# Performance work log

Hardware: AMD Instinct MI355X
Metric: run time of the kernel (lower is better)

The kernel has to match this reference:

```python
import jax, jax.numpy as jnp
import numpy as np


def _gru_layer(x_seq, W_ih, W_hh, b_ih, b_hh):
    """PyTorch-semantics GRU layer. x_seq: [T, B, in]. Returns outputs [T, B, H]."""
    H = W_hh.shape[1]
    # Precompute input projections for all timesteps: [T, B, 3H]
    xg = jnp.einsum('tbi,gi->tbg', x_seq, W_ih) + b_ih

    def step(h, xg_t):
        hg = h @ W_hh.T + b_hh                      # [B, 3H]
        xr, xz, xn = jnp.split(xg_t, 3, axis=-1)    # gate order: r, z, n
        hr, hz, hn = jnp.split(hg, 3, axis=-1)
        r = jax.nn.sigmoid(xr + hr)
        z = jax.nn.sigmoid(xz + hz)
        n = jnp.tanh(xn + r * hn)
        h_new = (1.0 - z) * n + z * h
        return h_new, h_new

    h0 = jnp.zeros((x_seq.shape[1], H), dtype=x_seq.dtype)
    _, out = jax.lax.scan(step, h0, xg)
    return out


def setup_inputs() -> dict:
    key = jax.random.key(0)
    ks = jax.random.split(key, 12)
    T, B, I, H, O = 128, 2048, 18, 256, 4
    s = 0.05  # small init scale to avoid gate saturation
    return {
        'x':     jax.random.normal(ks[0], (T, B, I), dtype=jnp.float32),
        'W_ih0': jax.random.normal(ks[1], (3 * H, I), dtype=jnp.float32) * s,
        'W_hh0': jax.random.normal(ks[2], (3 * H, H), dtype=jnp.float32) * s,
        'b_ih0': jax.random.normal(ks[3], (3 * H,), dtype=jnp.float32) * s,
        'b_hh0': jax.random.normal(ks[4], (3 * H,), dtype=jnp.float32) * s,
        'W_ih1': jax.random.normal(ks[5], (3 * H, H), dtype=jnp.float32) * s,
        'W_hh1': jax.random.normal(ks[6], (3 * H, H), dtype=jnp.float32) * s,
        'b_ih1': jax.random.normal(ks[7], (3 * H,), dtype=jnp.float32) * s,
        'b_hh1': jax.random.normal(ks[8], (3 * H,), dtype=jnp.float32) * s,
        'fc_w':  jax.random.normal(ks[9], (O, H), dtype=jnp.float32) * s,
        'fc_b':  jax.random.normal(ks[10], (O,), dtype=jnp.float32) * s,
    }


def reference(x, W_ih0, W_hh0, b_ih0, b_hh0, W_ih1, W_hh1, b_ih1, b_hh1, fc_w, fc_b):
    h1 = _gru_layer(x, W_ih0, W_hh0, b_ih0, b_hh0)   # [T, B, H]
    h2 = _gru_layer(h1, W_ih1, W_hh1, b_ih1, b_hh1)  # [T, B, H]
    logits = h2[-1] @ fc_w.T + fc_b                  # [B, O]
    return jax.nn.sigmoid(logits) * 2.0 - 1.0
```

## Files before the change

### kernel.cpp

```cpp
#include <hip/hip_runtime.h>
#include <hip/hip_bf16.h>
#include <stdint.h>

#define T_STEPS 128
#define BATCH   2048
#define IN_DIM  18
#define HID     256

#define NT   48
#define KT0  9
#define KT1  16
#define L0_FRAGS 432
#define L1_FRAGS 768
#define TOT_FRAGS 1200

#define CNT_OFF  1310720u
#define CNTA(g)  (CNT_OFF + (uint32_t)(g) * 64u)
#define CNTB(g)  (CNT_OFF + 4096u + (uint32_t)(g) * 64u)
#define CNTC(g)  (CNT_OFF + 8192u + (uint32_t)(g) * 64u)
#define H1_OFF   1441792u
#define H1SLOT(t, g) (H1_OFF + (uint32_t)(((((t) & 3) * 64) + (g)) * 16384))
#define XG_OFF   5898240u
#define XGSLOT(t, g) (XG_OFF + (uint32_t)(((((t) & 3) * 64) + (g)) * 49152))

#define XGOFFS(col, inner) ((uint32_t)((col) * 64 + ((inner) ^ (((col) & 7) << 3))))

using frag_ab = __attribute__((ext_vector_type(8))) short;
using f32x4   = __attribute__((ext_vector_type(4))) float;
using uint4v  = __attribute__((ext_vector_type(4))) unsigned int;
using uint2v  = __attribute__((ext_vector_type(2))) unsigned int;

__device__ __forceinline__ unsigned short f2bf(float f) {
  unsigned int u = __float_as_uint(f);
  u = (u + 0x7fffu + ((u >> 16) & 1u)) >> 16;
  return (unsigned short)u;
}
__device__ __forceinline__ float bf2f(unsigned short v) {
  return __uint_as_float((uint32_t)v << 16);
}
__device__ __forceinline__ float sigmoidf_(float v) {
  return __builtin_amdgcn_rcpf(1.f + __expf(-v));
}
__device__ __forceinline__ float tanhf_(float v) {
  float a = fabsf(v);
  float e = __expf(-2.f * a);
  float r = (1.f - e) * __builtin_amdgcn_rcpf(1.f + e);
  return v < 0.f ? -r : r;
}
__device__ __forceinline__ f32x4 mfma16(frag_ab a, frag_ab b, f32x4 c) {
  return __builtin_amdgcn_mfma_f32_16x16x32_bf16(a, b, c, 0, 0, 0);
}

__global__ __launch_bounds__(256) void repack_w(
    const float* __restrict__ Wih0, const float* __restrict__ Whh0,
    const float* __restrict__ Wih1, const float* __restrict__ Whh1,
    unsigned short* __restrict__ wq)
{
  int g = blockIdx.x * 256 + threadIdx.x;
  if (g >= TOT_FRAGS * 64) return;
  int f = g >> 6;
  int L = g & 63;
  int q = L >> 4, c16 = L & 15;
  unsigned short v[8];
  if (f < L0_FRAGS) {
    int n = f / KT0, kt = f - n * KT0;
    int col = n * 16 + c16;
    if (kt == 0) {
      #pragma unroll
      for (int j = 0; j < 8; ++j) {
        int k = q * 8 + j;
        v[j] = (k < IN_DIM) ? f2bf(Wih0[col * IN_DIM + k]) : (unsigned short)0;
      }
    } else {
      int kb = (kt - 1) * 32 + q * 8;
      #pragma unroll
      for (int j = 0; j < 8; ++j) v[j] = f2bf(Whh0[col * HID + kb + j]);
    }
  } else {
    int f1 = f - L0_FRAGS;
    int n = f1 / KT1, kt = f1 - n * KT1;
    int col = n * 16 + c16;
    const float* __restrict__ W = (kt < 8) ? Wih1 : Whh1;
    int kb = (kt & 7) * 32 + q * 8;
    #pragma unroll
    for (int j = 0; j < 8; ++j) v[j] = f2bf(W[col * HID + kb + j]);
  }
  frag_ab pv;
  #pragma unroll
  for (int j = 0; j < 8; ++j) pv[j] = (short)v[j];
  *(frag_ab*)((char*)wq + ((size_t)f << 10) + (size_t)(L << 4)) = pv;
}

__global__ __launch_bounds__(256) void clear_cnt(uint32_t* __restrict__ c) {
  int i = blockIdx.x * 256 + threadIdx.x;
  if (i < 3072) c[i] = 0;
}

__global__ __launch_bounds__(1024) void gru_pipe(
    const float* __restrict__ x,
    const float* __restrict__ bih0, const float* __restrict__ bhh0,
    const float* __restrict__ bih1, const float* __restrict__ bhh1,
    const float* __restrict__ fcw,  const float* __restrict__ fcb,
    char* __restrict__ ws,
    float* __restrict__ out)
{
  __shared__ __align__(16) char smem[82944];

  const int tid  = threadIdx.x;
  const int wave = tid >> 6;
  const int lane = tid & 63;
  const int q    = lane >> 4;
  const int c16  = lane & 15;
  const int bid  = blockIdx.x;
  const uint32_t lane16 = (uint32_t)(lane << 4);
  int dead = 0;

#define BARRIER() asm volatile("s_waitcnt lgkmcnt(0)\n\ts_barrier" ::: "memory")
#define ISSUE3(sl, oR, oZ, oN)                                              \
  asm volatile("global_load_dwordx4 %0, %3, %6\n\t"                         \
               "global_load_dwordx4 %1, %4, %6\n\t"                         \
               "global_load_dwordx4 %2, %5, %6"                             \
               : "=&v"(rr_[sl]), "=&v"(rz_[sl]), "=&v"(rn_[sl])             \
               : "v"((uint32_t)(oR)), "v"((uint32_t)(oZ)),                  \
                 "v"((uint32_t)(oN)), "s"(ws)                               \
               : "memory")
#define WAIT3(sl, NSTR)                                                     \
  asm volatile("s_waitcnt vmcnt(" NSTR ")"                                  \
               : "+v"(rr_[sl]), "+v"(rz_[sl]), "+v"(rn_[sl]) :: "memory")
#define SCLOAD4(dst, off)                                                   \
  asm volatile("global_load_dwordx4 %0, %1, %2 sc0 sc1"                     \
               : "=&v"(dst) : "v"((uint32_t)(off)), "s"(ws) : "memory")
#define SCSTORE4(off, val)                                                  \
  asm volatile("global_store_dwordx4 %0, %1, %2 sc0 sc1"                    \
               :: "v"((uint32_t)(off)), "v"(val), "s"(ws) : "memory")
#define SCSTORE2(off, val)                                                  \
  asm volatile("global_store_dwordx2 %0, %1, %2 sc0 sc1"                    \
               :: "v"((uint32_t)(off)), "v"(val), "s"(ws) : "memory")
#define PUBLISH(off, val)                                                   \
  asm volatile("global_store_dword %0, %1, %2 sc0 sc1"                      \
               :: "v"((uint32_t)(off)), "v"((uint32_t)(val)), "s"(ws)       \
               : "memory")
#define POLL(off, target)                                                   \
  do {                                                                      \
    int tgt = (target);                                                     \
    if (tgt > 0) {                                                          \
      int it = 0, bound = dead ? 64 : (1 << 17);                            \
      for (;;) {                                                            \
        uint32_t v_;                                                        \
        asm volatile("global_load_dword %0, %1, %2 sc0 sc1\n\t"             \
                     "s_waitcnt vmcnt(0)"                                   \
                     : "=&v"(v_) : "v"((uint32_t)(off)), "s"(ws)            \
                     : "memory");                                           \
        if ((int)v_ >= tgt) break;                                          \
        if (++it >= bound) { dead = 1; break; }                             \
        __builtin_amdgcn_s_sleep(2);                                        \
      }                                                                     \
    }                                                                       \
  } while (0)

  if (bid < 64) {
    const int g = bid, row0 = g * 32;
    unsigned short (*h1b)[264] = (unsigned short (*)[264])smem;
    unsigned short (*xs)[32]   = (unsigned short (*)[32])(smem + 33792);
    for (int i = tid; i < 2 * 32 * 264; i += 1024) ((unsigned short*)smem)[i] = 0;
    for (int i = tid; i < 2 * 32 * 32; i += 1024) ((unsigned short*)(smem + 33792))[i] = 0;
    const int c = wave * 16 + c16;
    const float brc = bih0[c] + bhh0[c];
    const float bzc = bih0[HID + c] + bhh0[HID + c];
    const float bni = bih0[2 * HID + c];
    const float bnh = bhh0[2 * HID + c];
    {
      int r = tid & 31, cc = tid >> 5;
      float xv = x[(size_t)(row0 + r) * IN_DIM + (cc < 18 ? cc : 17)];
      if (cc < 18) xs[r][cc] = f2bf(xv);
    }
    __syncthreads();

    const uint32_t b0r = (uint32_t)((wave * KT0) << 10);
    const uint32_t b0z = (uint32_t)(((16 + wave) * KT0) << 10);
    const uint32_t b0n = (uint32_t)(((32 + wave) * KT0) << 10);
    frag_ab rr_[3], rz_[3], rn_[3];
    float h1m[2][4] = {{0, 0, 0, 0}, {0, 0, 0, 0}};
    uint32_t xvu = 0;
    #pragma unroll
    for (int i = 0; i < 3; ++i)
      ISSUE3(i, b0r + i * 1024 + lane16, b0z + i * 1024 + lane16,
                b0n + i * 1024 + lane16);

    for (int t = 0; t < T_STEPS; ++t) {
      const int p = t & 1, pn = p ^ 1;
      {
        int t1 = (t + 1 < T_STEPS) ? t + 1 : T_STEPS - 1;
        int r = tid & 31, cc = tid >> 5;
        uint32_t xo = (uint32_t)((((t1 * BATCH) + row0 + r) * IN_DIM +
                                  (cc < 18 ? cc : 17)) * 4);
        asm volatile("global_load_dword %0, %1, %2"
                     : "=&v"(xvu) : "v"(xo), "s"(x) : "memory");
      }
      f32x4 a_r[2] = {{0,0,0,0},{0,0,0,0}}, a_z[2] = {{0,0,0,0},{0,0,0,0}};
      f32x4 a_nx[2] = {{0,0,0,0},{0,0,0,0}}, a_nh[2] = {{0,0,0,0},{0,0,0,0}};
      #pragma unroll
      for (int i = 0; i < KT0; ++i) {
        const int sl = i % 3;
        WAIT3(sl, "6");
        frag_ab A0, A1v;
        if (i == 0) {
          A0  = *(const frag_ab*)&xs[p * 32 + c16][q * 8];
          A1v = *(const frag_ab*)&xs[p * 32 + 16 + c16][q * 8];
        } else {
          A0  = *(const frag_ab*)&h1b[p * 32 + c16][(i - 1) * 32 + q * 8];
          A1v = *(const frag_ab*)&h1b[p * 32 + 16 + c16][(i - 1) * 32 + q * 8];
        }
        a_r[0] = mfma16(A0, rr_[sl], a_r[0]);  a_r[1] = mfma16(A1v, rr_[sl], a_r[1]);
        a_z[0] = mfma16(A0, rz_[sl], a_z[0]);  a_z[1] = mfma16(A1v, rz_[sl], a_z[1]);
        if (i == 0) { a_nx[0] = mfma16(A0, rn_[sl], a_nx[0]);
                      a_nx[1] = mfma16(A1v, rn_[sl], a_nx[1]); }
        else        { a_nh[0] = mfma16(A0, rn_[sl], a_nh[0]);
                      a_nh[1] = mfma16(A1v, rn_[sl], a_nh[1]); }
        const int nk = (i + 3) % KT0;
        ISSUE3(sl, b0r + nk * 1024 + lane16, b0z + nk * 1024 + lane16,
                   b0n + nk * 1024 + lane16);
      }
      { int r = tid & 31, cc = tid >> 5;
        if (cc < 18) xs[pn * 32 + r][cc] = f2bf(__uint_as_float(xvu)); }
      #pragma unroll
      for (int mt = 0; mt < 2; ++mt)
        #pragma unroll
        for (int rrI = 0; rrI < 4; ++rrI) {
          const int row = mt * 16 + q * 4 + rrI;
          float rg = sigmoidf_(a_r[mt][rrI] + brc);
          float zg = sigmoidf_(a_z[mt][rrI] + bzc);
          float ng = tanhf_(a_nx[mt][rrI] + bni + rg * (a_nh[mt][rrI] + bnh));
          float hn = (1.f - zg) * ng + zg * h1m[mt][rrI];
          h1m[mt][rrI] = hn;
          h1b[pn * 32 + row][c] = f2bf(hn);
        }
      BARRIER();
      {
        const int mt = wave >> 3, kt = wave & 7;
        frag_ab fa = *(const frag_ab*)&h1b[pn * 32 + mt * 16 + c16][kt * 32 + q * 8];
        SCSTORE4(H1SLOT(t, g) + (uint32_t)(wave * 1024 + lane * 16), fa);
      }
      if (tid == 0) POLL(CNTB(g), t - 3);
      asm volatile("s_waitcnt vmcnt(0)" ::: "memory");
      BARRIER();
      if (tid == 0) PUBLISH(CNTA(g), t + 1);
    }

  } else if (bid < 128) {
    const int g = bid - 64;
    unsigned short* slab = (unsigned short*)smem;
    const int c = wave * 16 + c16;
    const float bri = bih1[c], bzi = bih1[HID + c], bni = bih1[2 * HID + c];
    const uint32_t b1r = (uint32_t)((L0_FRAGS + wave * KT1) << 10);
    const uint32_t b1z = (uint32_t)((L0_FRAGS + (16 + wave) * KT1) << 10);
    const uint32_t b1n = (uint32_t)((L0_FRAGS + (32 + wave) * KT1) << 10);
    frag_ab rr_[4], rz_[4], rn_[4];
    #pragma unroll
    for (int i = 0; i < 4; ++i)
      ISSUE3(i, b1r + i * 1024 + lane16, b1z + i * 1024 + lane16,
                b1n + i * 1024 + lane16);

    if (tid == 0) POLL(CNTA(g), 1);
    BARRIER();
    { uint4v u; SCLOAD4(u, H1SLOT(0, g) + tid * 16);
      asm volatile("s_waitcnt vmcnt(0)" : "+v"(u) :: "memory");
      *(uint4v*)((char*)slab + tid * 16) = u; }
    if (tid == 0) POLL(CNTA(g), 2);
    __syncthreads();

    for (int t = 0; t < T_STEPS; ++t) {
      const int p = t & 1, pn = p ^ 1;
      uint4v stg = {0, 0, 0, 0};
      const bool hasst = (t + 1 < T_STEPS);
      if (hasst) SCLOAD4(stg, H1SLOT(t + 1, g) + tid * 16);
      f32x4 acc[3][2];
      #pragma unroll
      for (int ga = 0; ga < 3; ++ga) { acc[ga][0] = (f32x4){0,0,0,0};
                                       acc[ga][1] = (f32x4){0,0,0,0}; }
      #pragma unroll
      for (int i = 0; i < 8; ++i) {
        const int sl = i & 3;
        WAIT3(sl, "9");
        frag_ab A0  = *(const frag_ab*)((char*)slab + p * 16384 + (i * 64 + lane) * 16);
        frag_ab A1v = *(const frag_ab*)((char*)slab + p * 16384 + ((8 + i) * 64 + lane) * 16);
        acc[0][0] = mfma16(A0, rr_[sl], acc[0][0]); acc[0][1] = mfma16(A1v, rr_[sl], acc[0][1]);
        acc[1][0] = mfma16(A0, rz_[sl], acc[1][0]); acc[1][1] = mfma16(A1v, rz_[sl], acc[1][1]);
        acc[2][0] = mfma16(A0, rn_[sl], acc[2][0]); acc[2][1] = mfma16(A1v, rn_[sl], acc[2][1]);
        const int nk = (i + 4) & 7;
        ISSUE3(sl, b1r + nk * 1024 + lane16, b1z + nk * 1024 + lane16,
                   b1n + nk * 1024 + lane16);
      }
      if (hasst) *(uint4v*)((char*)slab + pn * 16384 + tid * 16) = stg;
      #pragma unroll
      for (int ga = 0; ga < 3; ++ga) {
        const float bb = (ga == 0) ? bri : (ga == 1) ? bzi : bni;
        const int col = ga * 256 + c;
        #pragma unroll
        for (int mt = 0; mt < 2; ++mt) {
          uint2v u;
          u[0] = (uint32_t)f2bf(acc[ga][mt][0] + bb) |
                 ((uint32_t)f2bf(acc[ga][mt][1] + bb) << 16);
          u[1] = (uint32_t)f2bf(acc[ga][mt][2] + bb) |
                 ((uint32_t)f2bf(acc[ga][mt][3] + bb) << 16);
          SCSTORE2(XGSLOT(t, g) + XGOFFS(col, (mt * 16 + q * 4) * 2), u);
        }
      }
      if (tid == 0) {
        if (t <= 125) POLL(CNTA(g), t + 3);
        POLL(CNTC(g), t - 3);
      }
      asm volatile("s_waitcnt vmcnt(0)" ::: "memory");
      BARRIER();
      if (tid == 0) PUBLISH(CNTB(g), t + 1);
    }

  } else {
    const int g = bid - 128, row0 = g * 32;
    unsigned short* xg = (unsigned short*)smem;
    unsigned short (*h2b)[264] = (unsigned short (*)[264])(smem + 49152);
    for (int i = tid; i < 2 * 32 * 264; i += 1024)
      ((unsigned short*)(smem + 49152))[i] = 0;
    const int c = wave * 16 + c16;
    const float brh = bhh1[c], bzh = bhh1[HID + c], bnh = bhh1[2 * HID + c];
    const uint32_t bCr = (uint32_t)((L0_FRAGS + wave * KT1 + 8) << 10);
    const uint32_t bCz = (uint32_t)((L0_FRAGS + (16 + wave) * KT1 + 8) << 10);
    const uint32_t bCn = (uint32_t)((L0_FRAGS + (32 + wave) * KT1 + 8) << 10);
    frag_ab rr_[4], rz_[4], rn_[4];
    float h2m[2][4] = {{0, 0, 0, 0}, {0, 0, 0, 0}};
    #pragma unroll
    for (int i = 0; i < 4; ++i)
      ISSUE3(i, bCr + i * 1024 + lane16, bCz + i * 1024 + lane16,
                bCn + i * 1024 + lane16);

    if (tid == 0) POLL(CNTB(g), 1);
    BARRIER();
    { uint4v u0, u1, u2;
      SCLOAD4(u0, XGSLOT(0, g) + tid * 16);
      SCLOAD4(u1, XGSLOT(0, g) + 16384 + tid * 16);
      SCLOAD4(u2, XGSLOT(0, g) + 32768 + tid * 16);
      asm volatile("s_waitcnt vmcnt(0)" : "+v"(u0), "+v"(u1), "+v"(u2) :: "memory");
      *(uint4v*)((char*)xg + tid * 16) = u0;
      *(uint4v*)((char*)xg + 16384 + tid * 16) = u1;
      *(uint4v*)((char*)xg + 32768 + tid * 16) = u2; }
    if (tid == 0) POLL(CNTB(g), 2);
    __syncthreads();

    for (int t = 0; t < T_STEPS; ++t) {
      const int p = t & 1, pn = p ^ 1;
      uint4v s0 = {0,0,0,0}, s1 = {0,0,0,0}, s2 = {0,0,0,0};
      const bool hasst = (t + 1 < T_STEPS);
      if (hasst) {
        SCLOAD4(s0, XGSLOT(t + 1, g) + tid * 16);
        SCLOAD4(s1, XGSLOT(t + 1, g) + 16384 + tid * 16);
        SCLOAD4(s2, XGSLOT(t + 1, g) + 32768 + tid * 16);
      }
      f32x4 acc[3][2];
      #pragma unroll
      for (int ga = 0; ga < 3; ++ga) { acc[ga][0] = (f32x4){0,0,0,0};
                                       acc[ga][1] = (f32x4){0,0,0,0}; }
      #pragma unroll
      for (int i = 0; i < 8; ++i) {
        const int sl = i & 3;
        WAIT3(sl, "9");
        frag_ab A0  = *(const frag_ab*)&h2b[p * 32 + c16][i * 32 + q * 8];
        frag_ab A1v = *(const frag_ab*)&h2b[p * 32 + 16 + c16][i * 32 + q * 8];
        acc[0][0] = mfma16(A0, rr_[sl], acc[0][0]); acc[0][1] = mfma16(A1v, rr_[sl], acc[0][1]);
        acc[1][0] = mfma16(A0, rz_[sl], acc[1][0]); acc[1][1] = mfma16(A1v, rz_[sl], acc[1][1]);
        acc[2][0] = mfma16(A0, rn_[sl], acc[2][0]); acc[2][1] = mfma16(A1v, rn_[sl], acc[2][1]);
        const int nk = (i + 4) & 7;
        ISSUE3(sl, bCr + nk * 1024 + lane16, bCz + nk * 1024 + lane16,
                   bCn + nk * 1024 + lane16);
      }
      #pragma unroll
      for (int mt = 0; mt < 2; ++mt) {
        uint2v ur = *(const uint2v*)((char*)xg + XGOFFS(0 * 256 + c, (mt * 16 + q * 4) * 2));
        uint2v uz = *(const uint2v*)((char*)xg + XGOFFS(1 * 256 + c, (mt * 16 + q * 4) * 2));
        uint2v un = *(const uint2v*)((char*)xg + XGOFFS(2 * 256 + c, (mt * 16 + q * 4) * 2));
        #pragma unroll
        for (int rrI = 0; rrI < 4; ++rrI) {
          const int row = mt * 16 + q * 4 + rrI;
          const uint32_t wr = (rrI < 2) ? ur[0] : ur[1];
          const uint32_t wz = (rrI < 2) ? uz[0] : uz[1];
          const uint32_t wn = (rrI < 2) ? un[0] : un[1];
          const int sh = (rrI & 1) * 16;
          float xr = bf2f((unsigned short)(wr >> sh));
          float xz = bf2f((unsigned short)(wz >> sh));
          float xn = bf2f((unsigned short)(wn >> sh));
          float rg = sigmoidf_(xr + acc[0][mt][rrI] + brh);
          float zg = sigmoidf_(xz + acc[1][mt][rrI] + bzh);
          float ng = tanhf_(xn + rg * (acc[2][mt][rrI] + bnh));
          float hn = (1.f - zg) * ng + zg * h2m[mt][rrI];
          h2m[mt][rrI] = hn;
          h2b[pn * 32 + row][c] = f2bf(hn);
        }
      }
      BARRIER();
      if (tid == 0 && t <= 125) POLL(CNTB(g), t + 3);
      if (hasst) {
        asm volatile("s_waitcnt vmcnt(0)" : "+v"(s0), "+v"(s1), "+v"(s2) :: "memory");
        *(uint4v*)((char*)xg + tid * 16) = s0;
        *(uint4v*)((char*)xg + 16384 + tid * 16) = s1;
        *(uint4v*)((char*)xg + 32768 + tid * 16) = s2;
      }
      BARRIER();
      if (tid == 0) PUBLISH(CNTC(g), t + 1);
    }

    if (tid < 128) {
      const int row = tid >> 2, o = tid & 3;
      float acc2 = fcb[o];
      #pragma unroll 8
      for (int k = 0; k < HID; ++k)
        acc2 += bf2f(h2b[row][k]) * fcw[o * HID + k];
      float sg = sigmoidf_(acc2);
      out[(size_t)(row0 + row) * 4 + o] = sg * 2.f - 1.f;
    }
  }
#undef BARRIER
#undef ISSUE3
#undef WAIT3
#undef SCLOAD4
#undef SCSTORE4
#undef SCSTORE2
#undef PUBLISH
#undef POLL
}

extern "C" void kernel_launch(void* const* d_in, const int* in_sizes, int n_in,
                              void* d_out, int out_size, void* d_ws, size_t ws_size,
                              hipStream_t stream) {
  const float* x    = (const float*)d_in[0];
  const float* Wih0 = (const float*)d_in[1];
  const float* Whh0 = (const float*)d_in[2];
  const float* bih0 = (const float*)d_in[3];
  const float* bhh0 = (const float*)d_in[4];
  const float* Wih1 = (const float*)d_in[5];
  const float* Whh1 = (const float*)d_in[6];
  const float* bih1 = (const float*)d_in[7];
  const float* bhh1 = (const float*)d_in[8];
  const float* fcw  = (const float*)d_in[9];
  const float* fcb  = (const float*)d_in[10];

  unsigned short* wq = (unsigned short*)d_ws;
  uint32_t* cnt = (uint32_t*)((char*)d_ws + CNT_OFF);

  repack_w<<<(TOT_FRAGS * 64 + 255) / 256, 256, 0, stream>>>(Wih0, Whh0, Wih1, Whh1, wq);
  clear_cnt<<<12, 256, 0, stream>>>(cnt);
  gru_pipe<<<192, 1024, 0, stream>>>(x, bih0, bhh0, bih1, bhh1, fcw, fcb,
                                     (char*)d_ws, (float*)d_out);
}
```

Baseline: 803.6 us.

## Keep two W_ih1 k-tiles register-resident in the layer-1 input-projection blocks

In the layer-1 input-projection blocks, the first two k-tiles of the r/z/n weights are loaded once into registers and kept for the whole time loop. Only the remaining six k-tiles are streamed through a three-slot ring each step, with adjusted vmcnt waits. This cuts per-step global/L2 weight traffic but raises VGPR pressure, and the launch bound now asks for a minimum occupancy. The float-to-bf16 conversion also switches from round-to-nearest-even to a simpler round-half-up, which slightly changes rounding.

```diff
diff --git a/kernel.cpp b/kernel.cpp
--- a/kernel.cpp
+++ b/kernel.cpp
@@ -31,9 +31,7 @@
 using uint2v  = __attribute__((ext_vector_type(2))) unsigned int;
 
 __device__ __forceinline__ unsigned short f2bf(float f) {
-  unsigned int u = __float_as_uint(f);
-  u = (u + 0x7fffu + ((u >> 16) & 1u)) >> 16;
-  return (unsigned short)u;
+  return (unsigned short)((__float_as_uint(f) + 0x8000u) >> 16);
 }
 __device__ __forceinline__ float bf2f(unsigned short v) {
   return __uint_as_float((uint32_t)v << 16);
@@ -96,7 +94,7 @@
   if (i < 3072) c[i] = 0;
 }
 
-__global__ __launch_bounds__(1024) void gru_pipe(
+__global__ __launch_bounds__(1024, 4) void gru_pipe(
     const float* __restrict__ x,
     const float* __restrict__ bih0, const float* __restrict__ bhh0,
     const float* __restrict__ bih1, const float* __restrict__ bhh1,
@@ -127,6 +125,9 @@
 #define WAIT3(sl, NSTR)                                                     \
   asm volatile("s_waitcnt vmcnt(" NSTR ")"                                  \
                : "+v"(rr_[sl]), "+v"(rz_[sl]), "+v"(rn_[sl]) :: "memory")
+#define RESLOAD(dst, off)                                                   \
+  asm volatile("global_load_dwordx4 %0, %1, %2"                             \
+               : "=&v"(dst) : "v"((uint32_t)(off)), "s"(ws) : "memory")
 #define SCLOAD4(dst, off)                                                   \
   asm volatile("global_load_dwordx4 %0, %1, %2 sc0 sc1"                     \
                : "=&v"(dst) : "v"((uint32_t)(off)), "s"(ws) : "memory")
@@ -255,11 +256,22 @@
     const uint32_t b1r = (uint32_t)((L0_FRAGS + wave * KT1) << 10);
     const uint32_t b1z = (uint32_t)((L0_FRAGS + (16 + wave) * KT1) << 10);
     const uint32_t b1n = (uint32_t)((L0_FRAGS + (32 + wave) * KT1) << 10);
-    frag_ab rr_[4], rz_[4], rn_[4];
-    #pragma unroll
-    for (int i = 0; i < 4; ++i)
-      ISSUE3(i, b1r + i * 1024 + lane16, b1z + i * 1024 + lane16,
-                b1n + i * 1024 + lane16);
+    frag_ab rr_[3], rz_[3], rn_[3];
+    frag_ab w_r0, w_r1, w_z0, w_z1, w_n0, w_n1;
+    RESLOAD(w_r0, b1r + 0 * 1024 + lane16);
+    RESLOAD(w_r1, b1r + 1 * 1024 + lane16);
+    RESLOAD(w_z0, b1z + 0 * 1024 + lane16);
+    RESLOAD(w_z1, b1z + 1 * 1024 + lane16);
+    RESLOAD(w_n0, b1n + 0 * 1024 + lane16);
+    RESLOAD(w_n1, b1n + 1 * 1024 + lane16);
+    asm volatile("s_waitcnt vmcnt(3)"
+                 : "+v"(w_r0), "+v"(w_r1), "+v"(w_z0) :: "memory");
+    asm volatile("s_waitcnt vmcnt(0)"
+                 : "+v"(w_z1), "+v"(w_n0), "+v"(w_n1) :: "memory");
+    __builtin_amdgcn_sched_barrier(0);
+    ISSUE3(0, b1r + 2 * 1024 + lane16, b1z + 2 * 1024 + lane16, b1n + 2 * 1024 + lane16);
+    ISSUE3(1, b1r + 3 * 1024 + lane16, b1z + 3 * 1024 + lane16, b1n + 3 * 1024 + lane16);
+    ISSUE3(2, b1r + 4 * 1024 + lane16, b1z + 4 * 1024 + lane16, b1n + 4 * 1024 + lane16);
 
     if (tid == 0) POLL(CNTA(g), 1);
     BARRIER();
@@ -279,17 +291,31 @@
       for (int ga = 0; ga < 3; ++ga) { acc[ga][0] = (f32x4){0,0,0,0};
                                        acc[ga][1] = (f32x4){0,0,0,0}; }
       #pragma unroll
-      for (int i = 0; i < 8; ++i) {
-        const int sl = i & 3;
-        WAIT3(sl, "9");
-        frag_ab A0  = *(const frag_ab*)((char*)slab + p * 16384 + (i * 64 + lane) * 16);
-        frag_ab A1v = *(const frag_ab*)((char*)slab + p * 16384 + ((8 + i) * 64 + lane) * 16);
+      for (int js = 0; js < 6; ++js) {
+        const int kt = 2 + js, sl = js % 3;
+        if (js < 3) { WAIT3(sl, "9"); } else { WAIT3(sl, "6"); }
+        frag_ab A0  = *(const frag_ab*)((char*)slab + p * 16384 + (kt * 64 + lane) * 16);
+        frag_ab A1v = *(const frag_ab*)((char*)slab + p * 16384 + ((8 + kt) * 64 + lane) * 16);
         acc[0][0] = mfma16(A0, rr_[sl], acc[0][0]); acc[0][1] = mfma16(A1v, rr_[sl], acc[0][1]);
         acc[1][0] = mfma16(A0, rz_[sl], acc[1][0]); acc[1][1] = mfma16(A1v, rz_[sl], acc[1][1]);
         acc[2][0] = mfma16(A0, rn_[sl], acc[2][0]); acc[2][1] = mfma16(A1v, rn_[sl], acc[2][1]);
-        const int nk = (i + 4) & 7;
-        ISSUE3(sl, b1r + nk * 1024 + lane16, b1z + nk * 1024 + lane16,
-                   b1n + nk * 1024 + lane16);
+        const int ktn = (js < 3) ? kt + 3 : kt - 3;
+        ISSUE3(sl, b1r + ktn * 1024 + lane16, b1z + ktn * 1024 + lane16,
+                   b1n + ktn * 1024 + lane16);
+      }
+      {
+        frag_ab A0  = *(const frag_ab*)((char*)slab + p * 16384 + (0 * 64 + lane) * 16);
+        frag_ab A1v = *(const frag_ab*)((char*)slab + p * 16384 + (8 * 64 + lane) * 16);
+        acc[0][0] = mfma16(A0, w_r0, acc[0][0]); acc[0][1] = mfma16(A1v, w_r0, acc[0][1]);
+        acc[1][0] = mfma16(A0, w_z0, acc[1][0]); acc[1][1] = mfma16(A1v, w_z0, acc[1][1]);
+        acc[2][0] = mfma16(A0, w_n0, acc[2][0]); acc[2][1] = mfma16(A1v, w_n0, acc[2][1]);
+      }
+      {
+        frag_ab A0  = *(const frag_ab*)((char*)slab + p * 16384 + (1 * 64 + lane) * 16);
+        frag_ab A1v = *(const frag_ab*)((char*)slab + p * 16384 + (9 * 64 + lane) * 16);
+        acc[0][0] = mfma16(A0, w_r1, acc[0][0]); acc[0][1] = mfma16(A1v, w_r1, acc[0][1]);
+        acc[1][0] = mfma16(A0, w_z1, acc[1][0]); acc[1][1] = mfma16(A1v, w_z1, acc[1][1]);
+        acc[2][0] = mfma16(A0, w_n1, acc[2][0]); acc[2][1] = mfma16(A1v, w_n1, acc[2][1]);
       }
       if (hasst) *(uint4v*)((char*)slab + pn * 16384 + tid * 16) = stg;
       #pragma unroll
@@ -420,6 +446,7 @@
 #undef BARRIER
 #undef ISSUE3
 #undef WAIT3
+#undef RESLOAD
 #undef SCLOAD4
 #undef SCSTORE4
 #undef SCSTORE2
```

Result: faster. 786.7 us (-2.1%).
